# Optimization experiments

Hardware: AMD Instinct MI355X
Metric: run time of the kernel (lower is better)

## Reference

```python
import jax, jax.numpy as jnp
import numpy as np

N = 100000      # nodes
E = 3200000     # edges (avg degree 32)
F_IN = 500      # input features
HID = 8         # per-head hidden dim (layer 1)
HEADS = 8       # heads (layer 1)
NC = 41         # num classes (layer 2, 1 head)


def setup_inputs() -> dict:
    key = jax.random.key(0)
    ks = jax.random.split(key, 8)
    x = jax.random.normal(ks[0], (N, F_IN), jnp.float32)
    edge_index = jax.random.randint(ks[1], (2, E), 0, N, dtype=jnp.int64)
    W1 = jax.random.normal(ks[2], (F_IN, HEADS * HID), jnp.float32) / np.sqrt(F_IN)
    a1_src = jax.random.normal(ks[3], (HEADS, HID), jnp.float32) / np.sqrt(HID)
    a1_dst = jax.random.normal(ks[4], (HEADS, HID), jnp.float32) / np.sqrt(HID)
    W2 = jax.random.normal(ks[5], (HEADS * HID, NC), jnp.float32) / np.sqrt(HEADS * HID)
    a2_src = jax.random.normal(ks[6], (1, NC), jnp.float32) / np.sqrt(NC)
    a2_dst = jax.random.normal(ks[7], (1, NC), jnp.float32) / np.sqrt(NC)
    return {"x": x, "edge_index": edge_index, "W1": W1, "a1_src": a1_src,
            "a1_dst": a1_dst, "W2": W2, "a2_src": a2_src, "a2_dst": a2_dst}


def gat_layer(x, edge_index, W, a_src, a_dst, heads, out_dim, concat):
    n = x.shape[0]
    h = (x @ W).reshape(n, heads, out_dim)                    # [N,H,D]
    # per-node attention halves (avoids gathering full features for logits)
    alpha_src = jnp.einsum('nhd,hd->nh', h, a_src)            # [N,H]
    alpha_dst = jnp.einsum('nhd,hd->nh', h, a_dst)            # [N,H]
    src, dst = edge_index[0], edge_index[1]
    e = jax.nn.leaky_relu(alpha_src[src] + alpha_dst[dst], 0.2)  # [E,H]
    # segment softmax over incoming edges of each destination node
    e_max = jax.lax.stop_gradient(jax.ops.segment_max(e, dst, num_segments=n))
    e_exp = jnp.exp(e - e_max[dst])
    denom = jax.ops.segment_sum(e_exp, dst, num_segments=n)
    alpha = e_exp / (denom[dst] + 1e-16)                      # [E,H]
    msg = alpha[:, :, None] * h[src]                          # [E,H,D]
    out = jax.ops.segment_sum(msg, dst, num_segments=n)       # [N,H,D]
    return out.reshape(n, heads * out_dim) if concat else out.mean(axis=1)


def reference(x, edge_index, W1, a1_src, a1_dst, W2, a2_src, a2_dst):
    # dropout layers are identity at inference
    h = gat_layer(x, edge_index, W1, a1_src, a1_dst, HEADS, HID, True)   # [N,64]
    h = jax.nn.elu(h)
    out = gat_layer(h, edge_index, W2, a2_src, a2_dst, 1, NC, False)     # [N,41]
    return jax.nn.log_softmax(out, axis=1)
```

## Files before the change

### kernel.cpp

```cpp
#include <hip/hip_runtime.h>
#include <hip/hip_bf16.h>
#include <math.h>


#define DEV __device__ __forceinline__

constexpr int N_NODES = 100000;
constexpr int N_EDGES = 3200000;
constexpr int F_IN    = 500;
constexpr int HEADS   = 8;
constexpr int HID     = 8;
constexpr int D1      = HEADS * HID;
constexpr int NC      = 41;
constexpr int NCP     = 64;

constexpr int NB    = 196;
constexpr int BCAP  = 20480;
constexpr int CSTR  = 16;
constexpr int SEPT  = 8;
constexpr int SCHUNK = 512 * SEPT;
constexpr int SBLKS = (N_EDGES + SCHUNK - 1) / SCHUNK;

constexpr int GROWS = 32;
constexpr int LROW  = 520;
constexpr int GBLKS = N_NODES / GROWS;

constexpr int WSTR = 68;

typedef __attribute__((ext_vector_type(8))) short bf16x8;
typedef __attribute__((ext_vector_type(4))) float f32x4;

DEV float bf2f(unsigned short u) {
    return __uint_as_float(((unsigned int)u) << 16);
}
DEV unsigned short f2b(float f) {
    unsigned int u = __float_as_uint(f);
    unsigned int r = (u + 0x7FFFu + ((u >> 16) & 1u)) >> 16;
    return (unsigned short)r;
}
DEV float leaky(float e) { return e > 0.f ? e : 0.2f * e; }
DEV float readlane_f(float v, int l) {
    return __uint_as_float((unsigned int)__builtin_amdgcn_readlane((int)__float_as_uint(v), l));
}

__global__ void k_detect(const void* xraw, const void* eraw, int* flags) {
    const int lane = threadIdx.x & 63;
    const unsigned short* xu = (const unsigned short*)xraw;
    unsigned short v = xu[2 * lane];
    int e = (v >> 7) & 0xFF;
    int valid = (e == 0 || (e >= 90 && e <= 150)) ? 1 : 0;
    unsigned long long vm = __ballot(valid);
    const unsigned int* eu = (const unsigned int*)eraw;
    unsigned long long zm = __ballot(eu[2 * lane + 1] == 0u);
    if (lane == 0) {
        flags[0] = (__popcll(vm) < 56) ? 1 : 0;
        flags[1] = (__popcll(zm) == 64) ? 1 : 0;
    }
}

__global__ __launch_bounds__(256) void k_convert(const void* w1, const void* a1s, const void* a1d,
                                                 const void* w2, const void* a2s, const void* a2d,
                                                 const int* flags,
                                                 unsigned short* W1frag, float* A1Sf, float* A1Df,
                                                 float* W2f, float* A2Sf, float* A2Df) {
    const bool f32 = flags[0] != 0;
    if (blockIdx.x == 0) {
        auto conv = [&](const void* src, float* dst, int n) {
            if (f32) {
                const float* s = (const float*)src;
                for (int i = threadIdx.x; i < n; i += blockDim.x) dst[i] = s[i];
            } else {
                const unsigned short* s = (const unsigned short*)src;
                for (int i = threadIdx.x; i < n; i += blockDim.x) dst[i] = bf2f(s[i]);
            }
        };
        conv(a1s, A1Sf, HEADS * HID);
        conv(a1d, A1Df, HEADS * HID);
        conv(w2, W2f, D1 * NC);
        conv(a2s, A2Sf, NC);
        conv(a2d, A2Df, NC);
    }
    for (int idx = blockIdx.x * 256 + threadIdx.x; idx < 4 * 16 * 64 * 8; idx += 64 * 256) {
        int wid = idx >> 13, kb = (idx >> 9) & 15, ln = (idx >> 3) & 63, j = idx & 7;
        int k = kb * 32 + (ln >> 4) * 8 + j;
        int n = wid * 16 + (ln & 15);
        unsigned short bits = 0;
        if (k < F_IN) {
            if (f32) bits = f2b(((const float*)w1)[k * D1 + n]);
            else     bits = ((const unsigned short*)w1)[k * D1 + n];
        }
        W1frag[idx] = bits;
    }
}

__global__ __launch_bounds__(512, 8) void k_gemm1_scat(const void* xraw, const void* eraw,
                                                       const int* flags,
                                                       const unsigned short* __restrict__ W1frag,
                                                       const float* A1Sf, const float* A1Df,
                                                       unsigned short* __restrict__ h1b,
                                                       float* __restrict__ as1,
                                                       float* __restrict__ ad1,
                                                       int* bucket_cnt, unsigned int* staging) {
    __shared__ unsigned short ldsx[GROWS * LROW];
    const int t = threadIdx.x;

    if (blockIdx.x < SBLKS) {
        int* hist  = (int*)ldsx;
        int* lbase = hist + 256;
        int* gbase = lbase + 256;
        unsigned char* pbk = (unsigned char*)(gbase + 196);
        unsigned* pay = (unsigned*)(pbk + 4096);

        const bool e64 = flags[1] != 0;
        const unsigned int* eu = (const unsigned int*)eraw;
        const int e0 = blockIdx.x * SCHUNK;
        const int total = min(SCHUNK, N_EDGES - e0);

        for (int i = t; i < 256; i += 512) hist[i] = 0;
        __syncthreads();

        int sv[SEPT], dv[SEPT];
#pragma unroll
        for (int k = 0; k < SEPT; k++) {
            int i = e0 + k * 512 + t;
            if (i < N_EDGES) {
                if (e64) { sv[k] = (int)eu[2 * i]; dv[k] = (int)eu[2 * (N_EDGES + i)]; }
                else     { sv[k] = (int)eu[i];     dv[k] = (int)eu[N_EDGES + i]; }
                atomicAdd(&hist[dv[k] >> 9], 1);
            } else dv[k] = -1;
        }
        __syncthreads();

        if (t < 256) lbase[t] = hist[t];
        __syncthreads();
        for (int o = 1; o < 256; o <<= 1) {
            int v = 0;
            if (t < 256 && t >= o) v = lbase[t - o];
            __syncthreads();
            if (t < 256) lbase[t] += v;
            __syncthreads();
        }
        if (t < NB) {
            int c = hist[t];
            int ex = lbase[t] - c;
            int base = c ? atomicAdd(&bucket_cnt[t * CSTR], c) : 0;
            lbase[t] = ex;
            gbase[t] = t * BCAP + base;
        }
        __syncthreads();
        if (t < NB) hist[t] = lbase[t];
        __syncthreads();

#pragma unroll
        for (int k = 0; k < SEPT; k++) {
            if (dv[k] >= 0) {
                int b = dv[k] >> 9;
                int slot = atomicAdd(&hist[b], 1);
                pay[slot] = (unsigned)sv[k] | ((unsigned)(dv[k] & 511) << 17);
                pbk[slot] = (unsigned char)b;
            }
        }
        __syncthreads();

        for (int j = t; j < total; j += 512) {
            int b = pbk[j];
            staging[gbase[b] + (j - lbase[b])] = pay[j];
        }
        return;
    }

    const int r0 = (blockIdx.x - SBLKS) * GROWS;
    const bool xf32 = flags[0] != 0;
#pragma unroll 4
    for (int it = 0; it < 8; it++) {
        int s = it * 512 + t;
        int row = s >> 7, c4 = s & 127;
        int row_g = r0 + row;
        ushort4 v = make_ushort4(0, 0, 0, 0);
        if (c4 < 125) {
            if (xf32) {
                float4 f = *(const float4*)((const float*)xraw + (size_t)row_g * F_IN + c4 * 4);
                v = make_ushort4(f2b(f.x), f2b(f.y), f2b(f.z), f2b(f.w));
            } else {
                v = *(const ushort4*)((const unsigned short*)xraw + (size_t)row_g * F_IN + c4 * 4);
            }
        }
        *(ushort4*)(ldsx + row * LROW + c4 * 4) = v;
    }
    __syncthreads();

    const int lane = t & 63;
    const int w = t >> 6;
    const int wid = __builtin_amdgcn_readfirstlane(w & 3);
    const int mb  = __builtin_amdgcn_readfirstlane(w >> 2);
    const int m = lane & 15, q = lane >> 4;
    f32x4 acc = {0.f, 0.f, 0.f, 0.f};
    const unsigned short* wf = W1frag + (size_t)wid * 8192;
    const unsigned short* arow = ldsx + (mb * 16 + m) * LROW + q * 8;
#pragma unroll 4
    for (int kb = 0; kb < 16; kb++) {
        bf16x8 b = *(const bf16x8*)(wf + (kb * 64 + lane) * 8);
        bf16x8 a = *(const bf16x8*)(arow + kb * 32);
        acc = __builtin_amdgcn_mfma_f32_16x16x32_bf16(a, b, acc, 0, 0, 0);
    }
    const int col = wid * 16 + m;
    const float a_s = A1Sf[col], a_d = A1Df[col];
    const int h = 2 * wid + (m >> 3);
#pragma unroll
    for (int reg = 0; reg < 4; reg++) {
        int gr = r0 + mb * 16 + q * 4 + reg;
        float vacc = acc[reg];
        h1b[(size_t)gr * D1 + col] = f2b(vacc);
        float ts = vacc * a_s, td = vacc * a_d;
        ts += __shfl_xor(ts, 1, 64); td += __shfl_xor(td, 1, 64);
        ts += __shfl_xor(ts, 2, 64); td += __shfl_xor(td, 2, 64);
        ts += __shfl_xor(ts, 4, 64); td += __shfl_xor(td, 4, 64);
        if ((lane & 7) == 0) {
            as1[gr * HEADS + h] = ts;
            ad1[gr * HEADS + h] = td;
        }
    }
}

__global__ void k_cscan(const int* bucket_cnt, int* cbase, int* off) {
    __shared__ int s[256];
    int t = threadIdx.x;
    s[t] = (t < NB) ? bucket_cnt[t * CSTR] : 0;
    __syncthreads();
    for (int o = 1; o < 256; o <<= 1) {
        int v = (t >= o) ? s[t - o] : 0;
        __syncthreads();
        s[t] += v;
        __syncthreads();
    }
    if (t < NB) cbase[t + 1] = s[t];
    if (t == 0) { cbase[0] = 0; off[N_NODES] = N_EDGES; }
}

__global__ __launch_bounds__(1024) void k_csr_build(const unsigned int* __restrict__ staging,
                                                    const int* __restrict__ bucket_cnt,
                                                    const int* __restrict__ cbase,
                                                    int* __restrict__ off, int* __restrict__ csr) {
    __shared__ int sdeg[512];
    __shared__ int scur[512];
    const int t = threadIdx.x;
    const int b = blockIdx.x;
    const int n0 = b << 9;
    const int start = b * BCAP;
    const int end = start + bucket_cnt[b * CSTR];
    const int base = cbase[b];
    if (t < 512) sdeg[t] = 0;
    __syncthreads();
    for (int i = start + t; i < end; i += 1024)
        atomicAdd(&sdeg[staging[i] >> 17], 1);
    __syncthreads();
    int d = (t < 512) ? sdeg[t] : 0;
    for (int o = 1; o < 512; o <<= 1) {
        int v = (t < 512 && t >= o) ? sdeg[t - o] : 0;
        __syncthreads();
        if (t < 512) sdeg[t] += v;
        __syncthreads();
    }
    if (t < 512) {
        int excl = sdeg[t] - d;
        if (n0 + t < N_NODES) off[n0 + t] = base + excl;
        scur[t] = base + excl;
    }
    __syncthreads();
    for (int i = start + t; i < end; i += 1024) {
        unsigned v = staging[i];
        int slot = atomicAdd(&scur[v >> 17], 1);
        csr[slot] = (int)(v & 0x1FFFFu);
    }
}

__global__ __launch_bounds__(256) void k_agg1(const int* __restrict__ csr,
                                              const int* __restrict__ off,
                                              const unsigned short* __restrict__ h1b,
                                              const float* __restrict__ as1,
                                              const float* __restrict__ ad1,
                                              float* __restrict__ h1e) {
    __shared__ float wlds[4][8 * WSTR];
    const int t = threadIdx.x;
    const int lane = t & 63;
    const int n = (blockIdx.x * blockDim.x + t) >> 6;
    if (n >= N_NODES) return;
    const int beg = off[n], end = off[n + 1];
    const int h0 = lane >> 3;
    float* wl = wlds[(t >> 6) & 3];
    const float* wrow = wl + h0 * WSTR;
    const float* adp = ad1 + n * HEADS;
    float acc = 0.f, dsum = 0.f;
    for (int base = beg; base < end; base += 64) {
        const int cnt = min(64, end - base);
        int sl = 0;
        if (lane < cnt) {
            sl = csr[base + lane];
            const float* ap = as1 + sl * HEADS;
            float4 aa = *(const float4*)(ap);
            float4 ab = *(const float4*)(ap + 4);
            wl[0 * WSTR + lane] = __expf(leaky(aa.x + adp[0]));
            wl[1 * WSTR + lane] = __expf(leaky(aa.y + adp[1]));
            wl[2 * WSTR + lane] = __expf(leaky(aa.z + adp[2]));
            wl[3 * WSTR + lane] = __expf(leaky(aa.w + adp[3]));
            wl[4 * WSTR + lane] = __expf(leaky(ab.x + adp[4]));
            wl[5 * WSTR + lane] = __expf(leaky(ab.y + adp[5]));
            wl[6 * WSTR + lane] = __expf(leaky(ab.z + adp[6]));
            wl[7 * WSTR + lane] = __expf(leaky(ab.w + adp[7]));
        }
        asm volatile("s_waitcnt lgkmcnt(0)" ::: "memory");
        int j = 0;
        for (; j + 4 <= cnt; j += 4) {
            int s0 = __builtin_amdgcn_readlane(sl, j);
            int s1 = __builtin_amdgcn_readlane(sl, j + 1);
            int s2 = __builtin_amdgcn_readlane(sl, j + 2);
            int s3 = __builtin_amdgcn_readlane(sl, j + 3);
            float4 wv = *(const float4*)(wrow + j);
            float g0 = bf2f(h1b[(size_t)s0 * D1 + lane]);
            float g1 = bf2f(h1b[(size_t)s1 * D1 + lane]);
            float g2 = bf2f(h1b[(size_t)s2 * D1 + lane]);
            float g3 = bf2f(h1b[(size_t)s3 * D1 + lane]);
            acc = fmaf(wv.x, g0, acc); dsum += wv.x;
            acc = fmaf(wv.y, g1, acc); dsum += wv.y;
            acc = fmaf(wv.z, g2, acc); dsum += wv.z;
            acc = fmaf(wv.w, g3, acc); dsum += wv.w;
        }
        for (; j < cnt; j++) {
            int s = __builtin_amdgcn_readlane(sl, j);
            float w = wrow[j];
            acc = fmaf(w, bf2f(h1b[(size_t)s * D1 + lane]), acc);
            dsum += w;
        }
    }
    float v = acc / (dsum + 1e-16f);
    float o = v > 0.f ? v : (__expf(v) - 1.f);
    h1e[(size_t)n * D1 + lane] = o;
}

__global__ __launch_bounds__(256) void k_gemm2(const float* __restrict__ h1e,
                                               const float* __restrict__ W2f,
                                               const float* __restrict__ A2Sf,
                                               const float* __restrict__ A2Df,
                                               unsigned short* __restrict__ h2p,
                                               float* __restrict__ as2,
                                               float* __restrict__ ad2) {
    const int row = blockIdx.x * blockDim.x + threadIdx.x;
    if (row >= N_NODES) return;
    float acc[NC];
#pragma unroll
    for (int c = 0; c < NC; c++) acc[c] = 0.f;
    const float* xr = h1e + (size_t)row * D1;
    for (int k = 0; k < D1; k += 4) {
        float4 hv = *(const float4*)(xr + k);
#pragma unroll
        for (int c = 0; c < NC; c++) {
            acc[c] = fmaf(hv.x, W2f[(k + 0) * NC + c], acc[c]);
            acc[c] = fmaf(hv.y, W2f[(k + 1) * NC + c], acc[c]);
            acc[c] = fmaf(hv.z, W2f[(k + 2) * NC + c], acc[c]);
            acc[c] = fmaf(hv.w, W2f[(k + 3) * NC + c], acc[c]);
        }
    }
    float ts = 0.f, td = 0.f;
#pragma unroll
    for (int c = 0; c < NC; c++) {
        h2p[(size_t)row * NCP + c] = f2b(acc[c]);
        ts = fmaf(acc[c], A2Sf[c], ts);
        td = fmaf(acc[c], A2Df[c], td);
    }
    as2[row] = ts;
    ad2[row] = td;
}

__global__ __launch_bounds__(256) void k_agg2(const int* __restrict__ csr,
                                              const int* __restrict__ off,
                                              const unsigned short* __restrict__ h2p,
                                              const float* __restrict__ as2,
                                              const float* __restrict__ ad2,
                                              const int* flags, void* out) {
    const int lane = threadIdx.x & 63;
    const int n = (blockIdx.x * blockDim.x + threadIdx.x) >> 6;
    if (n >= N_NODES) return;
    const int beg = off[n], end = off[n + 1];
    const float ad = ad2[n];
    const bool act = lane < NC;
    const int cl = act ? lane : 0;
    float acc = 0.f, dsum = 0.f;
    for (int base = beg; base < end; base += 64) {
        const int cnt = min(64, end - base);
        int idx = min(base + lane, N_EDGES - 1);
        int sl = csr[idx];
        float w = __expf(leaky(as2[sl] + ad));
        int j = 0;
        for (; j + 4 <= cnt; j += 4) {
            int s0 = __builtin_amdgcn_readlane(sl, j);
            int s1 = __builtin_amdgcn_readlane(sl, j + 1);
            int s2 = __builtin_amdgcn_readlane(sl, j + 2);
            int s3 = __builtin_amdgcn_readlane(sl, j + 3);
            float w0 = readlane_f(w, j);
            float w1 = readlane_f(w, j + 1);
            float w2 = readlane_f(w, j + 2);
            float w3 = readlane_f(w, j + 3);
            float g0 = bf2f(h2p[(size_t)s0 * NCP + cl]);
            float g1 = bf2f(h2p[(size_t)s1 * NCP + cl]);
            float g2 = bf2f(h2p[(size_t)s2 * NCP + cl]);
            float g3 = bf2f(h2p[(size_t)s3 * NCP + cl]);
            acc = fmaf(w0, g0, acc); dsum += w0;
            acc = fmaf(w1, g1, acc); dsum += w1;
            acc = fmaf(w2, g2, acc); dsum += w2;
            acc = fmaf(w3, g3, acc); dsum += w3;
        }
        for (; j < cnt; j++) {
            int s = __builtin_amdgcn_readlane(sl, j);
            float wj = readlane_f(w, j);
            acc = fmaf(wj, bf2f(h2p[(size_t)s * NCP + cl]), acc);
            dsum += wj;
        }
    }
    float val = acc / (dsum + 1e-16f);
    float v = act ? val : -INFINITY;
    float m = v;
#pragma unroll
    for (int o = 1; o < 64; o <<= 1) m = fmaxf(m, __shfl_xor(m, o, 64));
    float ex = act ? __expf(val - m) : 0.f;
#pragma unroll
    for (int o = 1; o < 64; o <<= 1) ex += __shfl_xor(ex, o, 64);
    float res = val - m - __logf(ex);
    if (act) {
        if (flags[0])
            ((float*)out)[(size_t)n * NC + lane] = res;
        else
            ((__hip_bfloat16*)out)[(size_t)n * NC + lane] = __float2bfloat16(res);
    }
}

extern "C" void kernel_launch(void* const* d_in, const int* in_sizes, int n_in,
                              void* d_out, int out_size, void* d_ws, size_t ws_size,
                              hipStream_t stream) {
    char* p = (char*)d_ws;
    auto alloc = [&](size_t bytes) -> void* {
        void* r = (void*)p;
        p += (bytes + 255) & ~(size_t)255;
        return r;
    };
    int* flags  = (int*)alloc(16);
    unsigned short* W1frag = (unsigned short*)alloc(4 * 16 * 64 * 8 * 2);
    float* A1Sf = (float*)alloc(HEADS * HID * 4);
    float* A1Df = (float*)alloc(HEADS * HID * 4);
    float* W2f  = (float*)alloc((size_t)D1 * NC * 4);
    float* A2Sf = (float*)alloc(NC * 4);
    float* A2Df = (float*)alloc(NC * 4);
    unsigned short* h1b = (unsigned short*)alloc((size_t)N_NODES * D1 * 2);
    float* as1  = (float*)alloc((size_t)N_NODES * HEADS * 4);
    float* ad1  = (float*)alloc((size_t)N_NODES * HEADS * 4);
    float* h1e  = (float*)alloc((size_t)N_NODES * D1 * 4);
    unsigned short* h2p = (unsigned short*)alloc((size_t)N_NODES * NCP * 2);
    float* as2  = (float*)alloc((size_t)N_NODES * 4);
    float* ad2  = (float*)alloc((size_t)N_NODES * 4);
    int* off    = (int*)alloc((size_t)(N_NODES + 1) * 4);
    int* csr    = (int*)alloc((size_t)N_EDGES * 4);
    int* bucket_cnt = (int*)alloc((size_t)NB * CSTR * 4);
    int* cbase      = (int*)alloc((size_t)(NB + 1) * 4);
    unsigned int* staging = (unsigned int*)h1e;

    hipMemsetAsync(bucket_cnt, 0, (size_t)NB * CSTR * 4, stream);

    k_detect<<<1, 64, 0, stream>>>(d_in[0], d_in[1], flags);
    k_convert<<<64, 256, 0, stream>>>(d_in[2], d_in[3], d_in[4], d_in[5], d_in[6], d_in[7],
                                      flags, W1frag, A1Sf, A1Df, W2f, A2Sf, A2Df);
    k_gemm1_scat<<<SBLKS + GBLKS, 512, 0, stream>>>(d_in[0], d_in[1], flags, W1frag,
                                                    A1Sf, A1Df, h1b, as1, ad1,
                                                    bucket_cnt, staging);
    k_cscan<<<1, 256, 0, stream>>>(bucket_cnt, cbase, off);
    k_csr_build<<<NB, 1024, 0, stream>>>(staging, bucket_cnt, cbase, off, csr);

    k_agg1<<<25000, 256, 0, stream>>>(csr, off, h1b, as1, ad1, h1e);
    k_gemm2<<<391, 256, 0, stream>>>(h1e, W2f, A2Sf, A2Df, h2p, as2, ad2);
    k_agg2<<<25000, 256, 0, stream>>>(csr, off, h2p, as2, ad2, flags, d_out);
}
```

Baseline: 593.3 us.

## Replace per-bucket CSR build with global degree scan and parallel fill

Per-node in-degrees are now counted with global atomics while edges are scattered. A three-kernel multi-block prefix scan turns them into offsets, and CSR fill is split into many smaller blocks per bucket that use global atomic cursors. This replaces the 196-block build that did a local histogram and scan inside each bucket, aiming for more parallelism in that phase. It costs 3.2M extra global atomics in the scatter kernel, plus global-atomic contention in the fill and two extra small launches. The convert kernel also gets more blocks.

```diff
diff --git a/kernel.cpp b/kernel.cpp
--- a/kernel.cpp
+++ b/kernel.cpp
@@ -20,6 +20,10 @@
 constexpr int SEPT  = 8;
 constexpr int SCHUNK = 512 * SEPT;
 constexpr int SBLKS = (N_EDGES + SCHUNK - 1) / SCHUNK;
+constexpr int FCHUNK = 4096;
+constexpr int FPB   = (BCAP + FCHUNK - 1) / FCHUNK;
+
+constexpr int SCBLK = (N_NODES + 1023) / 1024;
 
 constexpr int GROWS = 32;
 constexpr int LROW  = 520;
@@ -80,7 +84,7 @@
         conv(a2s, A2Sf, NC);
         conv(a2d, A2Df, NC);
     }
-    for (int idx = blockIdx.x * 256 + threadIdx.x; idx < 4 * 16 * 64 * 8; idx += 64 * 256) {
+    for (int idx = blockIdx.x * 256 + threadIdx.x; idx < 4 * 16 * 64 * 8; idx += 256 * 256) {
         int wid = idx >> 13, kb = (idx >> 9) & 15, ln = (idx >> 3) & 63, j = idx & 7;
         int k = kb * 32 + (ln >> 4) * 8 + j;
         int n = wid * 16 + (ln & 15);
@@ -100,7 +104,8 @@
                                                        unsigned short* __restrict__ h1b,
                                                        float* __restrict__ as1,
                                                        float* __restrict__ ad1,
-                                                       int* bucket_cnt, unsigned int* staging) {
+                                                       int* bucket_cnt, unsigned int* staging,
+                                                       int* __restrict__ deg) {
     __shared__ unsigned short ldsx[GROWS * LROW];
     const int t = threadIdx.x;
 
@@ -127,6 +132,7 @@
                 if (e64) { sv[k] = (int)eu[2 * i]; dv[k] = (int)eu[2 * (N_EDGES + i)]; }
                 else     { sv[k] = (int)eu[i];     dv[k] = (int)eu[N_EDGES + i]; }
                 atomicAdd(&hist[dv[k] >> 9], 1);
+                atomicAdd(&deg[dv[k]], 1);
             } else dv[k] = -1;
         }
         __syncthreads();
@@ -222,54 +228,68 @@
     }
 }
 
-__global__ void k_cscan(const int* bucket_cnt, int* cbase, int* off) {
-    __shared__ int s[256];
-    int t = threadIdx.x;
-    s[t] = (t < NB) ? bucket_cnt[t * CSTR] : 0;
+__global__ __launch_bounds__(1024) void k_scan1(const int* __restrict__ deg,
+                                                int* __restrict__ off, int* __restrict__ bsum) {
+    __shared__ int s[1024];
+    const int t = threadIdx.x;
+    const int n = blockIdx.x * 1024 + t;
+    int d = (n < N_NODES) ? deg[n] : 0;
+    s[t] = d;
     __syncthreads();
-    for (int o = 1; o < 256; o <<= 1) {
+    for (int o = 1; o < 1024; o <<= 1) {
         int v = (t >= o) ? s[t - o] : 0;
         __syncthreads();
         s[t] += v;
         __syncthreads();
     }
-    if (t < NB) cbase[t + 1] = s[t];
-    if (t == 0) { cbase[0] = 0; off[N_NODES] = N_EDGES; }
-}
-
-__global__ __launch_bounds__(1024) void k_csr_build(const unsigned int* __restrict__ staging,
-                                                    const int* __restrict__ bucket_cnt,
-                                                    const int* __restrict__ cbase,
-                                                    int* __restrict__ off, int* __restrict__ csr) {
-    __shared__ int sdeg[512];
-    __shared__ int scur[512];
+    if (n < N_NODES) off[n] = s[t] - d;
+    if (t == 1023) bsum[blockIdx.x] = s[1023];
+}
+
+__global__ __launch_bounds__(128) void k_scan2(const int* __restrict__ bsum,
+                                               int* __restrict__ bpre) {
+    __shared__ int s[128];
     const int t = threadIdx.x;
-    const int b = blockIdx.x;
+    int d = (t < SCBLK) ? bsum[t] : 0;
+    s[t] = d;
+    __syncthreads();
+    for (int o = 1; o < 128; o <<= 1) {
+        int v = (t >= o) ? s[t - o] : 0;
+        __syncthreads();
+        s[t] += v;
+        __syncthreads();
+    }
+    if (t < SCBLK) bpre[t] = s[t] - d;
+}
+
+__global__ __launch_bounds__(1024) void k_scan3(int* __restrict__ off,
+                                                const int* __restrict__ bpre,
+                                                int* __restrict__ cur) {
+    const int t = threadIdx.x;
+    const int n = blockIdx.x * 1024 + t;
+    if (n < N_NODES) {
+        int o = off[n] + bpre[blockIdx.x];
+        off[n] = o;
+        cur[n] = o;
+    }
+    if (n == 0) off[N_NODES] = N_EDGES;
+}
+
+__global__ __launch_bounds__(512) void k_csr_fill(const unsigned int* __restrict__ staging,
+                                                  const int* __restrict__ bucket_cnt,
+                                                  int* __restrict__ cur, int* __restrict__ csr) {
+    const int b = blockIdx.x / FPB;
+    const int c = blockIdx.x % FPB;
+    const int cnt = bucket_cnt[b * CSTR];
+    const int lo = c * FCHUNK;
+    if (lo >= cnt) return;
+    const int hi = min(cnt, lo + FCHUNK);
+    const int start = b * BCAP;
     const int n0 = b << 9;
-    const int start = b * BCAP;
-    const int end = start + bucket_cnt[b * CSTR];
-    const int base = cbase[b];
-    if (t < 512) sdeg[t] = 0;
-    __syncthreads();
-    for (int i = start + t; i < end; i += 1024)
-        atomicAdd(&sdeg[staging[i] >> 17], 1);
-    __syncthreads();
-    int d = (t < 512) ? sdeg[t] : 0;
-    for (int o = 1; o < 512; o <<= 1) {
-        int v = (t < 512 && t >= o) ? sdeg[t - o] : 0;
-        __syncthreads();
-        if (t < 512) sdeg[t] += v;
-        __syncthreads();
-    }
-    if (t < 512) {
-        int excl = sdeg[t] - d;
-        if (n0 + t < N_NODES) off[n0 + t] = base + excl;
-        scur[t] = base + excl;
-    }
-    __syncthreads();
-    for (int i = start + t; i < end; i += 1024) {
+    for (int i = start + lo + threadIdx.x; i < start + hi; i += 512) {
         unsigned v = staging[i];
-        int slot = atomicAdd(&scur[v >> 17], 1);
+        int node = n0 + (int)(v >> 17);
+        int slot = atomicAdd(&cur[node], 1);
         csr[slot] = (int)(v & 0x1FFFFu);
     }
 }
@@ -458,20 +478,26 @@
     float* ad2  = (float*)alloc((size_t)N_NODES * 4);
     int* off    = (int*)alloc((size_t)(N_NODES + 1) * 4);
     int* csr    = (int*)alloc((size_t)N_EDGES * 4);
+    int* deg    = (int*)alloc((size_t)N_NODES * 4);
+    int* cur    = (int*)alloc((size_t)N_NODES * 4);
+    int* bsum   = (int*)alloc((size_t)SCBLK * 4);
+    int* bpre   = (int*)alloc((size_t)SCBLK * 4);
     int* bucket_cnt = (int*)alloc((size_t)NB * CSTR * 4);
-    int* cbase      = (int*)alloc((size_t)(NB + 1) * 4);
     unsigned int* staging = (unsigned int*)h1e;
 
+    hipMemsetAsync(deg, 0, (size_t)N_NODES * 4, stream);
     hipMemsetAsync(bucket_cnt, 0, (size_t)NB * CSTR * 4, stream);
 
     k_detect<<<1, 64, 0, stream>>>(d_in[0], d_in[1], flags);
-    k_convert<<<64, 256, 0, stream>>>(d_in[2], d_in[3], d_in[4], d_in[5], d_in[6], d_in[7],
-                                      flags, W1frag, A1Sf, A1Df, W2f, A2Sf, A2Df);
+    k_convert<<<256, 256, 0, stream>>>(d_in[2], d_in[3], d_in[4], d_in[5], d_in[6], d_in[7],
+                                       flags, W1frag, A1Sf, A1Df, W2f, A2Sf, A2Df);
     k_gemm1_scat<<<SBLKS + GBLKS, 512, 0, stream>>>(d_in[0], d_in[1], flags, W1frag,
                                                     A1Sf, A1Df, h1b, as1, ad1,
-                                                    bucket_cnt, staging);
-    k_cscan<<<1, 256, 0, stream>>>(bucket_cnt, cbase, off);
-    k_csr_build<<<NB, 1024, 0, stream>>>(staging, bucket_cnt, cbase, off, csr);
+                                                    bucket_cnt, staging, deg);
+    k_scan1<<<SCBLK, 1024, 0, stream>>>(deg, off, bsum);
+    k_scan2<<<1, 128, 0, stream>>>(bsum, bpre);
+    k_scan3<<<SCBLK, 1024, 0, stream>>>(off, bpre, cur);
+    k_csr_fill<<<NB * FPB, 512, 0, stream>>>(staging, bucket_cnt, cur, csr);
 
     k_agg1<<<25000, 256, 0, stream>>>(csr, off, h1b, as1, ad1, h1e);
     k_gemm2<<<391, 256, 0, stream>>>(h1e, W2f, A2Sf, A2Df, h2p, as2, ad2);
```

Measured after the change: 828.6 us. 1.4x slower.
